# Kernel tuning notes

Hardware: AMD Instinct MI355X
Metric: run time of the kernel (lower is better)

Reference implementation:

```python
import jax, jax.numpy as jnp
import numpy as np

EPS = 1e-8


def _three_nn_interpolate(coords, ref_coords, features):
    # coords: [B, N, 3], ref_coords: [B, M, 3], features: [B, C, M]
    # squared pairwise distances [B, N, M]
    d2 = (
        jnp.sum(coords * coords, axis=-1, keepdims=True)          # [B, N, 1]
        + jnp.sum(ref_coords * ref_coords, axis=-1)[:, None, :]    # [B, 1, M]
        - 2.0 * jnp.einsum('bnd,bmd->bnm', coords, ref_coords)
    )
    neg_d, idx = jax.lax.top_k(-d2, 3)       # 3 nearest -> idx [B, N, 3]
    dist = -neg_d                             # squared dists of 3-NN
    w = 1.0 / (dist + EPS)
    w = w / jnp.sum(w, axis=-1, keepdims=True)  # [B, N, 3]
    feats_t = jnp.swapaxes(features, 1, 2)    # [B, M, C]
    gathered = jax.vmap(lambda f, i: f[i])(feats_t, idx)  # [B, N, 3, C]
    out = jnp.einsum('bnk,bnkc->bcn', w, gathered)         # [B, C, N]
    return out


def setup_inputs() -> dict:
    key = jax.random.key(0)
    ks = jax.random.split(key, 5)
    B, N, M = 2, 16384, 4096
    return {
        'coords': jax.random.normal(ks[0], (B, N, 3), dtype=jnp.float32),
        'ref_coords': jax.random.normal(ks[1], (B, M, 3), dtype=jnp.float32),
        'ref_features': jax.random.normal(ks[2], (B, 256, M), dtype=jnp.float32),
        'ref_t_embed': jax.random.normal(ks[3], (B, 128, M), dtype=jnp.float32),
        'points_features': jax.random.normal(ks[4], (B, 64, N), dtype=jnp.float32),
    }


def reference(coords, ref_coords, ref_features, ref_t_embed, points_features):
    # PointNetFPModule.forward: interpolate features and t_embed from the
    # coarse ref point set onto the dense point set, then concat skip features.
    features = _three_nn_interpolate(coords, ref_coords, ref_features)  # [B, 256, N]
    t_embed = _three_nn_interpolate(coords, ref_coords, ref_t_embed)    # [B, 128, N]
    features = jnp.concatenate([features, points_features], axis=1)     # [B, 320, N]
    return features, t_embed
```

## Files before the change

kernel.cpp:

```cpp
#include <hip/hip_runtime.h>
#include <cstdint>

#define BB 2
#define NN 16384
#define MM 4096
#define CF 256
#define CT 128
#define CP 64

#define TPB1 512
#define NPB1 32
#define CHUNK 2048
#define HALFE 1024

__global__ __launch_bounds__(TPB1, 8) void knn_kernel(
    const float* __restrict__ coords,
    const float* __restrict__ ref_coords,
    int4* __restrict__ wsI,
    float4* __restrict__ wsW)
{
#pragma clang fp contract(off)
    __shared__ float4 refs[CHUNK];
    __shared__ float  mD[NPB1][2][4];
    __shared__ int    mI[NPB1][2][4];

    const int tid = threadIdx.x;
    const int b   = blockIdx.y;
    const int n0  = blockIdx.x * NPB1;

    const int pl = (tid >> 3) & (NPB1 - 1);
    const int s  = tid & 7;
    const int h  = tid >> 8;
    const int n  = n0 + pl;

    const float* cp = coords + ((size_t)b * NN + n) * 3;
    const float cx = cp[0];
    const float cy = cp[1];
    const float cz = cp[2];
    const float cc = (cx * cx + cy * cy) + cz * cz;

    float d0 = INFINITY, d1 = INFINITY, d2v = INFINITY;
    int   i0 = 0, i1 = 0, i2 = 0;
    float tau = INFINITY;
    float thr = INFINITY;

    const float* rc = ref_coords + (size_t)b * MM * 3;

    for (int ch = 0; ch < MM / CHUNK; ++ch) {
        __syncthreads();
        for (int e = tid; e < CHUNK; e += TPB1) {
            const int j = ch * CHUNK + e;
            const float x = rc[3 * j + 0];
            const float y = rc[3 * j + 1];
            const float z = rc[3 * j + 2];
            refs[e] = make_float4(x + x, y + y, z + z, (x * x + y * y) + z * z);
        }
        __syncthreads();

        const int ebase = h * HALFE + s;
        const int jbase = ch * CHUNK + ebase;
        for (int it0 = 0; it0 < HALFE / 8; it0 += 32) {
            #pragma unroll 4
            for (int k = 0; k < 32; ++k) {
                const int off8 = (it0 + k) << 3;
                const float4 r = refs[ebase + off8];
                const float dot2 = (cx * r.x + cy * r.y) + cz * r.z;
                const float dd   = (cc + r.w) - dot2;
                if (__any(dd < thr)) {
                    const int j = jbase + off8;
                    const bool l2 = dd < d2v;
                    const bool l1 = dd < d1;
                    const bool l0 = dd < d0;
                    i2 = l2 ? (l1 ? i1 : j) : i2;
                    i1 = l1 ? (l0 ? i0 : j) : i1;
                    i0 = l0 ? j : i0;
                    const float n2  = __builtin_amdgcn_fmed3f(dd, d1, d2v);
                    const float n1  = __builtin_amdgcn_fmed3f(dd, d0, d1);
                    const float n0v = fminf(dd, d0);
                    d2v = n2; d1 = n1; d0 = n0v;
                    thr = fminf(d2v, tau);
                }
            }
            float tt = d2v;
            tt = fminf(tt, __shfl_xor(tt, 1, 64));
            tt = fminf(tt, __shfl_xor(tt, 2, 64));
            tt = fminf(tt, __shfl_xor(tt, 4, 64));
            tau = tt;
            thr = fminf(d2v, tau);
        }
    }

    auto ins = [&](float e, int f) {
        const bool l2 = (e < d2v) || (e == d2v && f < i2);
        const bool l1 = (e < d1)  || (e == d1  && f < i1);
        const bool l0 = (e < d0)  || (e == d0  && f < i0);
        d2v = l2 ? (l1 ? d1 : e) : d2v;  i2 = l2 ? (l1 ? i1 : f) : i2;
        d1  = l1 ? (l0 ? d0 : e) : d1;   i1 = l1 ? (l0 ? i0 : f) : i1;
        d0  = l0 ? e : d0;               i0 = l0 ? f : i0;
    };

    for (int off = 1; off < 8; off <<= 1) {
        const float e0 = __shfl_xor(d0,  off, 64);
        const float e1 = __shfl_xor(d1,  off, 64);
        const float e2 = __shfl_xor(d2v, off, 64);
        const int   f0 = __shfl_xor(i0,  off, 64);
        const int   f1 = __shfl_xor(i1,  off, 64);
        const int   f2 = __shfl_xor(i2,  off, 64);
        ins(e0, f0);
        ins(e1, f1);
        ins(e2, f2);
    }

    if (s == 0) {
        mD[pl][h][0] = d0;  mD[pl][h][1] = d1;  mD[pl][h][2] = d2v;
        mI[pl][h][0] = i0;  mI[pl][h][1] = i1;  mI[pl][h][2] = i2;
    }
    __syncthreads();

    if (h == 0 && s == 0) {
        ins(mD[pl][1][0], mI[pl][1][0]);
        ins(mD[pl][1][1], mI[pl][1][1]);
        ins(mD[pl][1][2], mI[pl][1][2]);
        float w0 = 1.0f / (d0  + 1e-8f);
        float w1 = 1.0f / (d1  + 1e-8f);
        float w2 = 1.0f / (d2v + 1e-8f);
        const float sum = (w0 + w1) + w2;
        wsI[(size_t)b * NN + n] = make_int4(i0, i1, i2, 0);
        wsW[(size_t)b * NN + n] = make_float4(w0 / sum, w1 / sum, w2 / sum, 0.0f);
    }
}

#define TPB2 512
#define NIB  (BB * (CF + CT) / 2)
#define NCB  32

__global__ __launch_bounds__(TPB2, 8) void interp_kernel(
    const float* __restrict__ refF,
    const float* __restrict__ refT,
    const float* __restrict__ pf,
    const int4*  __restrict__ wsI,
    const float4* __restrict__ wsW,
    float* __restrict__ out)
{
#pragma clang fp contract(off)
    __shared__ float rowA[MM];
    __shared__ float rowB[MM];
    const int tid  = threadIdx.x;
    const int task = blockIdx.x;
    const size_t outT_base = (size_t)BB * (CF + CP) * NN;

    if (task >= NIB) {
        const int t3 = task - NIB;
        for (int j = 0; j < 4; ++j) {
            const int r  = t3 * 4 + j;
            const int bb = r >> 6;
            const int c  = r & (CP - 1);
            const float4* s4 = (const float4*)(pf + ((size_t)bb * CP + c) * NN);
            float4* d4 = (float4*)(out + ((size_t)bb * (CF + CP) + CF + c) * NN);
            for (int i = tid; i < NN / 4; i += TPB2) d4[i] = s4[i];
        }
        return;
    }

    const int r0 = task * 2;
    const float* src0;
    float* dst0;
    int b;
    if (r0 < BB * CF) {
        b = r0 >> 8;
        const int c = r0 & (CF - 1);
        src0 = refF + ((size_t)b * CF + c) * MM;
        dst0 = out + ((size_t)b * (CF + CP) + c) * NN;
    } else {
        const int r2 = r0 - BB * CF;
        b = r2 >> 7;
        const int c = r2 & (CT - 1);
        src0 = refT + ((size_t)b * CT + c) * MM;
        dst0 = out + outT_base + ((size_t)b * CT + c) * NN;
    }
    const float* src1 = src0 + MM;
    float* dst1 = dst0 + NN;

    for (int i = tid; i < MM / 4; i += TPB2) {
        ((float4*)rowA)[i] = ((const float4*)src0)[i];
        ((float4*)rowB)[i] = ((const float4*)src1)[i];
    }
    __syncthreads();

    const int4*   wi = wsI + (size_t)b * NN;
    const float4* ww = wsW + (size_t)b * NN;

    auto clampi = [](int v) { return v < 0 ? 0 : (v > MM - 1 ? MM - 1 : v); };

    int4   id = wi[tid];
    float4 w  = ww[tid];
    for (int nq = tid; nq < NN; nq += TPB2) {
        const int nq2 = nq + TPB2;
        int4   idn;
        float4 wn;
        if (nq2 < NN) { idn = wi[nq2]; wn = ww[nq2]; }
        const int a0 = clampi(id.x), a1 = clampi(id.y), a2 = clampi(id.z);
        dst0[nq] = (w.x * rowA[a0] + w.y * rowA[a1]) + w.z * rowA[a2];
        dst1[nq] = (w.x * rowB[a0] + w.y * rowB[a1]) + w.z * rowB[a2];
        id = idn; w = wn;
    }
}

extern "C" void kernel_launch(void* const* d_in, const int* in_sizes, int n_in,
                              void* d_out, int out_size, void* d_ws, size_t ws_size,
                              hipStream_t stream) {
    const float* coords     = (const float*)d_in[0];
    const float* ref_coords = (const float*)d_in[1];
    const float* refF       = (const float*)d_in[2];
    const float* refT       = (const float*)d_in[3];
    const float* pf         = (const float*)d_in[4];
    float* out = (float*)d_out;

    int4*   wsI = (int4*)d_ws;
    float4* wsW = (float4*)((char*)d_ws + (size_t)BB * NN * sizeof(int4));

    hipLaunchKernelGGL(knn_kernel, dim3(NN / NPB1, BB), dim3(TPB1), 0, stream,
                       coords, ref_coords, wsI, wsW);
    hipLaunchKernelGGL(interp_kernel, dim3(NIB + NCB), dim3(TPB2), 0, stream,
                       refF, refT, pf, wsI, wsW, out);
}
```

Baseline: 180.4 us.

## Assign each query point to one 8-lane group scanning full ref chunk

```diff
diff --git a/kernel.cpp b/kernel.cpp
--- a/kernel.cpp
+++ b/kernel.cpp
@@ -9,11 +9,10 @@
 #define CP 64
 
 #define TPB1 512
-#define NPB1 32
+#define NPB1 64
 #define CHUNK 2048
-#define HALFE 1024
-
-__global__ __launch_bounds__(TPB1, 8) void knn_kernel(
+
+__global__ __launch_bounds__(TPB1, 4) void knn_kernel(
     const float* __restrict__ coords,
     const float* __restrict__ ref_coords,
     int4* __restrict__ wsI,
@@ -21,16 +20,13 @@
 {
 #pragma clang fp contract(off)
     __shared__ float4 refs[CHUNK];
-    __shared__ float  mD[NPB1][2][4];
-    __shared__ int    mI[NPB1][2][4];
 
     const int tid = threadIdx.x;
     const int b   = blockIdx.y;
     const int n0  = blockIdx.x * NPB1;
 
-    const int pl = (tid >> 3) & (NPB1 - 1);
+    const int pl = tid >> 3;
     const int s  = tid & 7;
-    const int h  = tid >> 8;
     const int n  = n0 + pl;
 
     const float* cp = coords + ((size_t)b * NN + n) * 3;
@@ -57,17 +53,16 @@
         }
         __syncthreads();
 
-        const int ebase = h * HALFE + s;
-        const int jbase = ch * CHUNK + ebase;
-        for (int it0 = 0; it0 < HALFE / 8; it0 += 32) {
+        const int jbase = ch * CHUNK;
+        for (int it0 = 0; it0 < CHUNK / 8; it0 += 32) {
             #pragma unroll 4
             for (int k = 0; k < 32; ++k) {
-                const int off8 = (it0 + k) << 3;
-                const float4 r = refs[ebase + off8];
+                const int e = s + ((it0 + k) << 3);
+                const float4 r = refs[e];
                 const float dot2 = (cx * r.x + cy * r.y) + cz * r.z;
                 const float dd   = (cc + r.w) - dot2;
                 if (__any(dd < thr)) {
-                    const int j = jbase + off8;
+                    const int j = jbase + e;
                     const bool l2 = dd < d2v;
                     const bool l1 = dd < d1;
                     const bool l0 = dd < d0;
@@ -76,16 +71,16 @@
                     i0 = l0 ? j : i0;
                     const float n2  = __builtin_amdgcn_fmed3f(dd, d1, d2v);
                     const float n1  = __builtin_amdgcn_fmed3f(dd, d0, d1);
-                    const float n0v = fminf(dd, d0);
-                    d2v = n2; d1 = n1; d0 = n0v;
+                    const float nv0 = fminf(dd, d0);
+                    d2v = n2; d1 = n1; d0 = nv0;
                     thr = fminf(d2v, tau);
                 }
             }
-            float tt = d2v;
-            tt = fminf(tt, __shfl_xor(tt, 1, 64));
-            tt = fminf(tt, __shfl_xor(tt, 2, 64));
-            tt = fminf(tt, __shfl_xor(tt, 4, 64));
-            tau = tt;
+            float t = d2v;
+            t = fminf(t, __shfl_xor(t, 1, 64));
+            t = fminf(t, __shfl_xor(t, 2, 64));
+            t = fminf(t, __shfl_xor(t, 4, 64));
+            tau = t;
             thr = fminf(d2v, tau);
         }
     }
@@ -112,15 +107,6 @@
     }
 
     if (s == 0) {
-        mD[pl][h][0] = d0;  mD[pl][h][1] = d1;  mD[pl][h][2] = d2v;
-        mI[pl][h][0] = i0;  mI[pl][h][1] = i1;  mI[pl][h][2] = i2;
-    }
-    __syncthreads();
-
-    if (h == 0 && s == 0) {
-        ins(mD[pl][1][0], mI[pl][1][0]);
-        ins(mD[pl][1][1], mI[pl][1][1]);
-        ins(mD[pl][1][2], mI[pl][1][2]);
         float w0 = 1.0f / (d0  + 1e-8f);
         float w1 = 1.0f / (d1  + 1e-8f);
         float w2 = 1.0f / (d2v + 1e-8f);
```

After: 160.7 us. 1.12x faster.
